# Kernel optimization log

Hardware: AMD Instinct MI355X
Metric: run time of the kernel (lower is better)

## Reference

```python
import jax, jax.numpy as jnp
import numpy as np

B, C, H, W = 4, 512, 96, 96
NH = 8
HD = C // NH
NC = 128
D = 768
L = H * W
EPS = 1e-5  # torch LayerNorm default


def _l2n(x, axis):
    # F.normalize: x / max(||x||, 1e-12)
    return x / jnp.maximum(jnp.linalg.norm(x, axis=axis, keepdims=True), 1e-12)


def _ln2d(x, g, b):
    # LayerNorm2d: normalize over channel dim of (B,C,H,W)
    mu = x.mean(1, keepdims=True)
    var = ((x - mu) ** 2).mean(1, keepdims=True)
    return (x - mu) / jnp.sqrt(var + EPS) * g[None, :, None, None] + b[None, :, None, None]


def _conv1x1(x, w):
    return jnp.einsum('oc,bchw->bohw', w, x)


def setup_inputs() -> dict:
    key = jax.random.key(0)
    ks = jax.random.split(key, 9)
    s = 0.02
    return {
        'img_feats': jax.random.normal(ks[0], (B, C, H, W), jnp.float32),
        'cls_embs': jax.random.normal(ks[1], (NC, D), jnp.float32),
        'cls_logits': jax.random.normal(ks[2], (B, NC), jnp.float32),
        'seg_logits': jax.random.normal(ks[3], (B, 1, H, W), jnp.float32),
        'gamma_g': jnp.ones((D,), jnp.float32), 'beta_g': jnp.zeros((D,), jnp.float32),
        'gamma_f': jnp.ones((C,), jnp.float32), 'beta_f': jnp.zeros((C,), jnp.float32),
        'attn_scale': jnp.ones((NH, 1, 1), jnp.float32),
        'Wg': jax.random.normal(ks[4], (C, D), jnp.float32) * s,
        'Wqkv': jax.random.normal(ks[5], (3 * C, C), jnp.float32) * s,
        'Wo': jax.random.normal(ks[6], (C, C), jnp.float32) * s,
        'bo': jnp.zeros((C,), jnp.float32),
        'gamma_n': jnp.ones((C,), jnp.float32), 'beta_n': jnp.zeros((C,), jnp.float32),
        'W1': jax.random.normal(ks[7], (C, C), jnp.float32) * s, 'b1': jnp.zeros((C,), jnp.float32),
        'W2': jax.random.normal(ks[8], (C, C), jnp.float32) * s, 'b2': jnp.zeros((C,), jnp.float32),
    }


def reference(img_feats, cls_embs, cls_logits, seg_logits, gamma_g, beta_g,
              gamma_f, beta_f, attn_scale, Wg, Wqkv, Wo, bo, gamma_n, beta_n,
              W1, b1, W2, b2):
    xn = _ln2d(img_feats, gamma_f, beta_f)
    # guide LayerNorm over embedding dim
    mu = cls_embs.mean(-1, keepdims=True)
    var = ((cls_embs - mu) ** 2).mean(-1, keepdims=True)
    cn = (cls_embs - mu) / jnp.sqrt(var + EPS) * gamma_g + beta_g
    g = (cn @ Wg.T).reshape(NC, NH, HD)  # nc nh hd

    qkv = _conv1x1(xn, Wqkv).reshape(B, 3, NH, HD, L)
    q, k, v = qkv[:, 0], qkv[:, 1], qkv[:, 2]  # each (B,NH,HD,L)

    # cosine guide map + min-max normalization + softmax-weighted aggregation over classes
    gm = jnp.einsum('nhd,bhdl->bhnl', _l2n(g, -1), _l2n(q, -2))
    gm = gm - gm.min(-1, keepdims=True)
    gm = gm / gm.max(-1, keepdims=True)
    gm = (jax.nn.softmax(gm, axis=2) * gm).sum(2, keepdims=True)  # (B,NH,1,L)

    # auxiliary guide map from cls logits + masked pooling of k
    cls_obj = jnp.einsum('nhd,bn->bhd', g, cls_logits)
    mask = jax.nn.sigmoid(seg_logits)  # (B,1,H,W)
    seg_obj = (mask * k.reshape(B, C, H, W)).sum((2, 3)) / mask.sum((2, 3))  # (B,C)
    obj = _l2n(cls_obj + seg_obj.reshape(B, NH, HD), -1)
    aux = jnp.einsum('bhd,bhdl->bhl', obj, _l2n(k, -2))[:, :, None, :]
    aux = aux - aux.min(-1, keepdims=True)
    aux = aux / aux.max(-1, keepdims=True)
    gm = gm * aux

    v = gm * v
    # channel (transposed) cosine attention: (B,NH,HD,HD)
    attn = jnp.einsum('bhdl,bhel->bhde', _l2n(q, -1), _l2n(k, -1)) * attn_scale
    out = jnp.einsum('bhde,bhel->bhdl', jax.nn.softmax(attn, -1), v).reshape(B, C, H, W)

    x = img_feats + _conv1x1(out, Wo) + bo[None, :, None, None]
    # ConvMlp with pre-norm: LayerNorm2d -> 1x1 conv -> GELU -> 1x1 conv
    fin = _ln2d(x, gamma_n, beta_n)
    h = jax.nn.gelu(_conv1x1(fin, W1) + b1[None, :, None, None], approximate=False)
    return x + _conv1x1(h, W2) + b2[None, :, None, None]
```

## Files before the change

### kernel.cpp

```cpp
#include <hip/hip_runtime.h>
#include <hip/hip_bf16.h>
#include <math.h>

#define BB 4
#define CC 512
#define NHEAD 8
#define HDIM 64
#define NCLS 128
#define DD 768
#define LL 9216
#define BLPIX 36864
#define EPSV 1e-5f
#define GMBLK 144
#define AUXBLK 36
#define LSPLIT 8
#define NLT 72

typedef __hip_bfloat16 bf16;
typedef __attribute__((ext_vector_type(8))) short short8v;
typedef __attribute__((ext_vector_type(4))) short short4v;
typedef __attribute__((ext_vector_type(4))) float f32x4;

__device__ __forceinline__ float bf2f(bf16 v){ return __bfloat162float(v); }
__device__ __forceinline__ bf16 f2bf(float v){ return __float2bfloat16(v); }
__device__ __forceinline__ short bfbits(float v){ bf16 b = __float2bfloat16(v); return *reinterpret_cast<short*>(&b); }
__device__ __forceinline__ float s2f(short s){ bf16 b = *reinterpret_cast<bf16*>(&s); return __bfloat162float(b); }

__global__ __launch_bounds__(256) void wclsg_k(
    const float* __restrict__ wqkv, const float* __restrict__ wo,
    const float* __restrict__ w1, const float* __restrict__ w2,
    bf16* __restrict__ oq, bf16* __restrict__ oo,
    bf16* __restrict__ o1, bf16* __restrict__ o2,
    const float* __restrict__ cls_embs, const float* __restrict__ gamma_g,
    const float* __restrict__ beta_g, const float* __restrict__ Wg,
    float* __restrict__ g, bf16* __restrict__ gnb)
{
  __shared__ __align__(16) float cn[DD];
  __shared__ float red[256];
  __shared__ float gsh[CC];
  __shared__ float nrm[NHEAD];
  int bid = blockIdx.x;
  int tid = threadIdx.x;
  if (bid < 1536){
    int i = bid * 256 + tid;
    int e = i * 4;
    const float* src; bf16* dst; int off;
    if (e < 786432){ src = wqkv; dst = oq; off = e; }
    else if (e < 1048576){ src = wo; dst = oo; off = e - 786432; }
    else if (e < 1310720){ src = w1; dst = o1; off = e - 1048576; }
    else { src = w2; dst = o2; off = e - 1310720; }
    float4 v = *reinterpret_cast<const float4*>(src + off);
    short4v pk;
    pk[0] = bfbits(v.x); pk[1] = bfbits(v.y); pk[2] = bfbits(v.z); pk[3] = bfbits(v.w);
    *(short4v*)&dst[off] = pk;
    return;
  }
  {
    int n = bid - 1536;
    const float* e = cls_embs + (size_t)n * DD;
    float s = 0.f, ss = 0.f;
    for (int i = tid; i < DD; i += 256){ float v = e[i]; s += v; ss += v * v; }
    red[tid] = s; __syncthreads();
    for (int st = 128; st > 0; st >>= 1){ if (tid < st) red[tid] += red[tid + st]; __syncthreads(); }
    float mean = red[0] / DD; __syncthreads();
    red[tid] = ss; __syncthreads();
    for (int st = 128; st > 0; st >>= 1){ if (tid < st) red[tid] += red[tid + st]; __syncthreads(); }
    float var = red[0] / DD - mean * mean;
    float rstd = rsqrtf(var + EPSV);
    __syncthreads();
    for (int i = tid; i < DD; i += 256) cn[i] = (e[i] - mean) * rstd * gamma_g[i] + beta_g[i];
    __syncthreads();
    for (int c = tid; c < CC; c += 256){
      const float* w = Wg + (size_t)c * DD;
      float a = 0.f;
      #pragma unroll 8
      for (int d = 0; d < DD; d++) a += cn[d] * w[d];
      gsh[c] = a;
    }
    __syncthreads();
    if (tid < NHEAD){
      float a = 0.f;
      for (int d = 0; d < HDIM; d++){ float v = gsh[tid * HDIM + d]; a += v * v; }
      nrm[tid] = fmaxf(sqrtf(a), 1e-12f);
    }
    __syncthreads();
    for (int c = tid; c < CC; c += 256){
      g[(size_t)n * CC + c] = gsh[c];
      gnb[(size_t)n * CC + c] = f2bf(gsh[c] / nrm[c >> 6]);
    }
  }
}

__global__ __launch_bounds__(256) void fuse_ln_k(const float* __restrict__ X,
    const float* __restrict__ lng, const float* __restrict__ lnb,
    bf16* __restrict__ xnT){
  __shared__ float sred[2][4][64];
  __shared__ float muS[64], rsS[64];
  __shared__ float t[64][65];
  int p0 = blockIdx.x * 64;
  int b = p0 / LL, l0 = p0 - b * LL;
  int tid = threadIdx.x;
  int cg = tid >> 6, l = tid & 63;
  const float* base = X + (size_t)b * CC * LL + l0 + l;
  float s = 0.f, ss = 0.f;
  for (int c = cg * 128; c < cg * 128 + 128; c++){
    float v = base[(size_t)c * LL];
    s += v; ss += v * v;
  }
  sred[0][cg][l] = s; sred[1][cg][l] = ss;
  __syncthreads();
  if (tid < 64){
    float st = sred[0][0][tid] + sred[0][1][tid] + sred[0][2][tid] + sred[0][3][tid];
    float sst = sred[1][0][tid] + sred[1][1][tid] + sred[1][2][tid] + sred[1][3][tid];
    float m = st * (1.0f / CC);
    float var = sst * (1.0f / CC) - m * m;
    muS[tid] = m; rsS[tid] = rsqrtf(var + EPSV);
  }
  __syncthreads();
  int pr = tid >> 4;
  int cc = (tid & 15) * 4;
  for (int cb = 0; cb < 8; cb++){
    int c0 = cb * 64;
    #pragma unroll
    for (int i = 0; i < 16; i++){
      int idx = i * 256 + tid;
      int cl = idx >> 6, ll2 = idx & 63;
      t[cl][ll2] = X[(size_t)b * CC * LL + (size_t)(c0 + cl) * LL + l0 + ll2];
    }
    __syncthreads();
    #pragma unroll
    for (int i = 0; i < 4; i++){
      int pl = pr + i * 16;
      int p = p0 + pl;
      float m = muS[pl], r = rsS[pl];
      short4v pk;
      #pragma unroll
      for (int e = 0; e < 4; e++){
        int c = c0 + cc + e;
        pk[e] = bfbits((t[cc + e][pl] - m) * r * lng[c] + lnb[c]);
      }
      *(short4v*)&xnT[(size_t)p * CC + c0 + cc] = pk;
    }
    __syncthreads();
  }
}

__global__ void statsred_k(const float2* __restrict__ statp, float* __restrict__ mu, float* __restrict__ rs){
  int p = blockIdx.x * 256 + threadIdx.x;
  if (p >= BLPIX) return;
  float s = 0.f, ss = 0.f;
  #pragma unroll
  for (int part = 0; part < 4; part++){
    float2 v = statp[part * BLPIX + p];
    s += v.x; ss += v.y;
  }
  float m = s * (1.0f / CC);
  float var = ss * (1.0f / CC) - m * m;
  mu[p] = m; rs[p] = rsqrtf(var + EPSV);
}

template<int MODE>
__global__ __launch_bounds__(256, 2) void mgemm_k(
    const bf16* __restrict__ A,
    const bf16* __restrict__ B,
    const float* __restrict__ residf,
    const bf16* __restrict__ residb,
    const float* __restrict__ bias,
    const float* __restrict__ mu, const float* __restrict__ rs,
    const float* __restrict__ lng, const float* __restrict__ lnb,
    float2* __restrict__ statp,
    float* __restrict__ qssp, float* __restrict__ kssp,
    bf16* __restrict__ qo, bf16* __restrict__ ko, bf16* __restrict__ vo,
    bf16* __restrict__ xT_out,
    float* __restrict__ xo,
    bf16* __restrict__ ho,
    const float* __restrict__ gA, const float* __restrict__ clsl, float* __restrict__ clsovO)
{
  __shared__ short Asm[128 * 64];
  __shared__ short Bsm[128 * 64];
  __shared__ float sredf[512];
  int tid = threadIdx.x;
  if (MODE == 0 && blockIdx.x >= 3456){
    int idx = (blockIdx.x - 3456) * 256 + tid;
    int b = idx >> 9, c = idx & 511;
    float a = 0.f;
    for (int n = 0; n < NCLS; n++) a += gA[(size_t)n * CC + c] * clsl[b * NCLS + n];
    clsovO[idx] = a;
    return;
  }
  int lane = tid & 63, wv = tid >> 6;
  int wr = wv >> 1, wc = wv & 1;
  int r15 = lane & 15, g = lane >> 4, h7 = lane & 7;
  int flat, gx, cpx;
  if (MODE == 0){ flat = blockIdx.x; gx = 12; cpx = 432; }
  else { gx = gridDim.x; flat = blockIdx.y * gx + blockIdx.x; cpx = (gx * gridDim.y) >> 3; }
  int swz = (flat & 7) * cpx + (flat >> 3);
  int m0 = (swz % gx) * 128, n0 = (swz / gx) * 128;
  int srow = tid >> 3, skkg = tid & 7;
  int sslot = ((skkg ^ (srow & 7))) * 8;

  f32x4 acc[4][4];
  #pragma unroll
  for (int i = 0; i < 4; i++)
    #pragma unroll
    for (int j = 0; j < 4; j++) acc[i][j] = (f32x4){0.f, 0.f, 0.f, 0.f};

  short8v pa[4], pb[4];
  auto loadAB = [&](int it){
    int k0 = it * 64;
    if (MODE == 2){
      int c0 = k0 + skkg * 8;
      float ga[8], be[8];
      *(float4*)&ga[0] = *(const float4*)&lng[c0];
      *(float4*)&ga[4] = *(const float4*)&lng[c0 + 4];
      *(float4*)&be[0] = *(const float4*)&lnb[c0];
      *(float4*)&be[4] = *(const float4*)&lnb[c0 + 4];
      #pragma unroll
      for (int r = 0; r < 4; r++){
        pa[r] = *reinterpret_cast<const short8v*>(A + (size_t)(m0 + r * 32 + srow) * 512 + c0);
        int rp = n0 + r * 32 + srow;
        float mm = mu[rp], rr = rs[rp];
        short8v rawv = *reinterpret_cast<const short8v*>(B + (size_t)rp * 512 + c0);
        short8v ov;
        #pragma unroll
        for (int e = 0; e < 8; e++){
          float v = (s2f(rawv[e]) - mm) * rr * ga[e] + be[e];
          ov[e] = bfbits(v);
        }
        pb[r] = ov;
      }
    } else {
      #pragma unroll
      for (int r = 0; r < 4; r++){
        pa[r] = *reinterpret_cast<const short8v*>(A + (size_t)(m0 + r * 32 + srow) * 512 + k0 + skkg * 8);
        pb[r] = *reinterpret_cast<const short8v*>(B + (size_t)(n0 + r * 32 + srow) * 512 + k0 + skkg * 8);
      }
    }
  };

  loadAB(0);
  for (int it = 0; it < 8; ++it){
    __syncthreads();
    #pragma unroll
    for (int r = 0; r < 4; r++){
      int row = r * 32 + srow;
      *(short8v*)&Asm[row * 64 + sslot] = pa[r];
      *(short8v*)&Bsm[row * 64 + sslot] = pb[r];
    }
    __syncthreads();
    if (it < 7) loadAB(it + 1);
    #pragma unroll
    for (int s = 0; s < 2; s++){
      int slot = ((s * 4 + g) ^ h7) * 8;
      short8v af[4], bf_[4];
      #pragma unroll
      for (int i = 0; i < 4; i++){
        af[i]  = *(const short8v*)&Asm[(wr * 64 + i * 16 + r15) * 64 + slot];
        bf_[i] = *(const short8v*)&Bsm[(wc * 64 + i * 16 + r15) * 64 + slot];
      }
      #pragma unroll
      for (int i = 0; i < 4; i++)
        #pragma unroll
        for (int j = 0; j < 4; j++){
          if (MODE == 2)
            acc[i][j] = __builtin_amdgcn_mfma_f32_16x16x32_bf16(bf_[i], af[j], acc[i][j], 0, 0, 0);
          else
            acc[i][j] = __builtin_amdgcn_mfma_f32_16x16x32_bf16(af[i], bf_[j], acc[i][j], 0, 0, 0);
        }
    }
  }

  int bIdx = n0 / LL;
  int lbase = n0 - bIdx * LL;
  if (MODE == 0){
    int part = m0 >> 9;
    if (part < 2){
      bf16* dst = (part == 0) ? qo : ko;
      int chb = (m0 & 511) + wr * 64;
      #pragma unroll
      for (int i = 0; i < 4; i++)
        #pragma unroll
        for (int j = 0; j < 4; j++){
          int l = lbase + wc * 64 + j * 16 + r15;
          #pragma unroll
          for (int e = 0; e < 4; e++){
            int ch = chb + i * 16 + g * 4 + e;
            dst[(size_t)bIdx * CC * LL + (size_t)ch * LL + l] = f2bf(acc[i][j][e]);
          }
        }
      #pragma unroll
      for (int i = 0; i < 4; i++)
        #pragma unroll
        for (int e = 0; e < 4; e++){
          float ssv = acc[i][0][e]*acc[i][0][e] + acc[i][1][e]*acc[i][1][e]
                    + acc[i][2][e]*acc[i][2][e] + acc[i][3][e]*acc[i][3][e];
          #pragma unroll
          for (int msk = 1; msk < 16; msk <<= 1) ssv += __shfl_xor(ssv, msk);
          if (r15 == 0) sredf[wv * 64 + i * 16 + g * 4 + e] = ssv;
        }
      __syncthreads();
      if (tid < 128){
        int wrr = tid >> 6, chL = tid & 63;
        float tot = sredf[(wrr * 2) * 64 + chL] + sredf[(wrr * 2 + 1) * 64 + chL];
        int c = (m0 & 511) + wrr * 64 + chL;
        int row = bIdx * 512 + c;
        int ltile = lbase >> 7;
        float* dd = (part == 0) ? qssp : kssp;
        dd[(size_t)row * NLT + ltile] = tot;
      }
    } else {
      int chb = (m0 & 511) + wr * 64;
      #pragma unroll
      for (int i = 0; i < 4; i++)
        #pragma unroll
        for (int j = 0; j < 4; j++){
          int l = lbase + wc * 64 + j * 16 + r15;
          int ch = chb + i * 16 + g * 4;
          short4v pk;
          #pragma unroll
          for (int e = 0; e < 4; e++) pk[e] = bfbits(acc[i][j][e]);
          *(short4v*)&vo[((size_t)bIdx * LL + l) * CC + ch] = pk;
        }
    }
  } else if (MODE == 1){
    float sj[4] = {0.f,0.f,0.f,0.f}, ssj[4] = {0.f,0.f,0.f,0.f};
    #pragma unroll
    for (int i = 0; i < 4; i++)
      #pragma unroll
      for (int j = 0; j < 4; j++){
        int l = lbase + wc * 64 + j * 16 + r15;
        int chm = m0 + wr * 64 + i * 16 + g * 4;
        short4v pk;
        #pragma unroll
        for (int e = 0; e < 4; e++){
          int m = chm + e;
          size_t o = (size_t)bIdx * CC * LL + (size_t)m * LL + l;
          float xv = residf[o] + acc[i][j][e] + bias[m];
          pk[e] = bfbits(xv);
          sj[j] += xv; ssj[j] += xv * xv;
        }
        *(short4v*)&xT_out[((size_t)bIdx * LL + l) * CC + chm] = pk;
      }
    #pragma unroll
    for (int j = 0; j < 4; j++){
      sj[j] += __shfl_xor(sj[j], 16); sj[j] += __shfl_xor(sj[j], 32);
      ssj[j] += __shfl_xor(ssj[j], 16); ssj[j] += __shfl_xor(ssj[j], 32);
    }
    if (g == 0){
      #pragma unroll
      for (int j = 0; j < 4; j++){
        sredf[wv * 128 + j * 32 + r15 * 2 + 0] = sj[j];
        sredf[wv * 128 + j * 32 + r15 * 2 + 1] = ssj[j];
      }
    }
    __syncthreads();
    if (tid < 128){
      int wv2 = tid >> 6, lane2 = tid & 63, j2 = lane2 >> 4, r2 = lane2 & 15;
      float s   = sredf[wv2 * 128 + j2 * 32 + r2 * 2 + 0] + sredf[(wv2 + 2) * 128 + j2 * 32 + r2 * 2 + 0];
      float ss2 = sredf[wv2 * 128 + j2 * 32 + r2 * 2 + 1] + sredf[(wv2 + 2) * 128 + j2 * 32 + r2 * 2 + 1];
      int p = n0 + wv2 * 64 + j2 * 16 + r2;
      statp[(m0 >> 7) * BLPIX + p] = make_float2(s, ss2);
    }
  } else if (MODE == 3){
    #pragma unroll
    for (int i = 0; i < 4; i++)
      #pragma unroll
      for (int j = 0; j < 4; j++){
        int l = lbase + wc * 64 + j * 16 + r15;
        int chm = m0 + wr * 64 + i * 16 + g * 4;
        short4v rv = *(const short4v*)&residb[((size_t)bIdx * LL + l) * CC + chm];
        #pragma unroll
        for (int e = 0; e < 4; e++){
          int m = chm + e;
          size_t o = (size_t)bIdx * CC * LL + (size_t)m * LL + l;
          xo[o] = s2f(rv[e]) + acc[i][j][e] + bias[m];
        }
      }
  } else {
    #pragma unroll
    for (int i = 0; i < 4; i++)
      #pragma unroll
      for (int j = 0; j < 4; j++){
        int mm = m0 + wr * 64 + j * 16 + r15;
        float bv = bias[mm];
        #pragma unroll
        for (int e = 0; e < 4; e++){
          int n = n0 + wc * 64 + i * 16 + g * 4 + e;
          float t = acc[i][j][e] + bv;
          float gv = 0.5f * t * (1.0f + erff(t * 0.70710678118654752f));
          ho[(size_t)n * CC + mm] = f2bf(gv);
        }
      }
  }
}

__global__ __launch_bounds__(256) void mega1_k(
    const bf16* __restrict__ q, const bf16* __restrict__ k, const bf16* __restrict__ gnb,
    float* __restrict__ pmin, float* __restrict__ pmax,
    float* __restrict__ part,
    const float* __restrict__ seg, float* __restrict__ seg_num, float* __restrict__ den,
    const float* __restrict__ qssp, const float* __restrict__ kssp,
    float* __restrict__ qn, float* __restrict__ kn)
{
  __shared__ __align__(16) char raw[9984];
  int bid = blockIdx.x;
  int t = threadIdx.x;
  if (bid < 4608){
    bf16* qs = (bf16*)raw;
    float (*sspart)[64] = (float(*)[64])(raw + 8704);
    float* rq = (float*)(raw + 8704 + 1024);
    int bh = bid & 31, lt = bid >> 5;
    int l0 = lt * 64;
    int b = bh >> 3, h = bh & 7;
    int w = t >> 6, lane = t & 63, r15 = lane & 15, g = lane >> 4;
    const bf16* qp = q + (size_t)b * CC * LL + (size_t)h * HDIM * LL + l0;
    #pragma unroll
    for (int i2 = 0; i2 < 4; i2++){
      int idx = t + i2 * 256;
      int d = idx >> 4, lch = (idx & 15) * 4;
      short4v vv = *reinterpret_cast<const short4v*>(qp + (size_t)d * LL + lch);
      *(short4v*)&qs[d * 68 + lch] = vv;
    }
    __syncthreads();
    {
      int l = t & 63, dg = t >> 6;
      float ss = 0.f;
      #pragma unroll
      for (int dd = 0; dd < 16; dd++){ float v = bf2f(qs[(dg * 16 + dd) * 68 + l]); ss += v * v; }
      sspart[dg][l] = ss;
    }
    __syncthreads();
    if (t < 64){
      float ss = sspart[0][t] + sspart[1][t] + sspart[2][t] + sspart[3][t];
      rq[t] = 1.0f / fmaxf(sqrtf(ss), 1e-12f);
    }
    __syncthreads();
    short8v ag[2][2];
    #pragma unroll
    for (int i = 0; i < 2; i++)
      #pragma unroll
      for (int kt = 0; kt < 2; kt++)
        ag[i][kt] = *reinterpret_cast<const short8v*>(gnb + (size_t)(w * 32 + i * 16 + r15) * CC + h * 64 + kt * 32 + g * 8);
    short8v bq[4][2];
    #pragma unroll
    for (int j = 0; j < 4; j++){
      float rqv = rq[j * 16 + r15];
      #pragma unroll
      for (int kt = 0; kt < 2; kt++){
        short8v bb;
        #pragma unroll
        for (int jj = 0; jj < 8; jj++){
          int d = kt * 32 + g * 8 + jj;
          bb[jj] = bfbits(bf2f(qs[d * 68 + j * 16 + r15]) * rqv);
        }
        bq[j][kt] = bb;
      }
    }
    f32x4 acc[2][4];
    #pragma unroll
    for (int i = 0; i < 2; i++)
      #pragma unroll
      for (int j = 0; j < 4; j++) acc[i][j] = (f32x4){0.f,0.f,0.f,0.f};
    #pragma unroll
    for (int kt = 0; kt < 2; kt++)
      #pragma unroll
      for (int i = 0; i < 2; i++)
        #pragma unroll
        for (int j = 0; j < 4; j++)
          acc[i][j] = __builtin_amdgcn_mfma_f32_16x16x32_bf16(ag[i][kt], bq[j][kt], acc[i][j], 0, 0, 0);
    #pragma unroll
    for (int i = 0; i < 2; i++)
      #pragma unroll
      for (int e = 0; e < 4; e++){
        float mn = acc[i][0][e], mx = acc[i][0][e];
        #pragma unroll
        for (int j = 1; j < 4; j++){ mn = fminf(mn, acc[i][j][e]); mx = fmaxf(mx, acc[i][j][e]); }
        #pragma unroll
        for (int msk = 1; msk < 16; msk <<= 1){
          mn = fminf(mn, __shfl_xor(mn, msk));
          mx = fmaxf(mx, __shfl_xor(mx, msk));
        }
        if (r15 == 0){
          int n = w * 32 + i * 16 + g * 4 + e;
          pmin[((size_t)bh * 128 + n) * GMBLK + lt] = mn;
          pmax[((size_t)bh * 128 + n) * GMBLK + lt] = mx;
        }
      }
    return;
  }
  if (bid < 4864){
    int bid2 = bid - 4608;
    int ls = bid2 & 7, bh = bid2 >> 3;
    int b = bh >> 3, h = bh & 7;
    int w = t >> 6, lane = t & 63, r15 = lane & 15, g = lane >> 4;
    const bf16* qp = q + (size_t)b * CC * LL + (size_t)h * HDIM * LL;
    const bf16* kp = k + (size_t)b * CC * LL + (size_t)h * HDIM * LL;
    int kbase = ls * 1152;
    f32x4 acc4[4];
    #pragma unroll
    for (int j = 0; j < 4; j++) acc4[j] = (f32x4){0.f,0.f,0.f,0.f};
    for (int ks = 0; ks < 36; ks++){
      int koff = kbase + ks * 32 + g * 8;
      short8v aq = *reinterpret_cast<const short8v*>(qp + (size_t)(w * 16 + r15) * LL + koff);
      short8v bk[4];
      #pragma unroll
      for (int j = 0; j < 4; j++) bk[j] = *reinterpret_cast<const short8v*>(kp + (size_t)(j * 16 + r15) * LL + koff);
      #pragma unroll
      for (int j = 0; j < 4; j++)
        acc4[j] = __builtin_amdgcn_mfma_f32_16x16x32_bf16(aq, bk[j], acc4[j], 0, 0, 0);
    }
    #pragma unroll
    for (int j = 0; j < 4; j++)
      #pragma unroll
      for (int e = 0; e < 4; e++){
        int d = w * 16 + g * 4 + e;
        int ee = j * 16 + r15;
        part[((size_t)(bh * LSPLIT + ls)) * 4096 + d * 64 + ee] = acc4[j][e];
      }
    return;
  }
  if (bid < 6912){
    float* red = (float*)raw;
    int bc = bid - 4864;
    int b = bc >> 9;
    const bf16* p = k + (size_t)bc * LL;
    const float* sp = seg + (size_t)b * LL;
    float s = 0.f;
    for (int i = t; i < LL; i += 256){
      float m = 1.0f / (1.0f + expf(-sp[i]));
      s += m * bf2f(p[i]);
    }
    red[t] = s; __syncthreads();
    for (int st = 128; st > 0; st >>= 1){ if (t < st) red[t] += red[t + st]; __syncthreads(); }
    if (t == 0) seg_num[bc] = red[0];
    return;
  }
  if (bid < 6916){
    float* red = (float*)raw;
    int b = bid - 6912;
    const float* sp = seg + (size_t)b * LL;
    float s = 0.f;
    for (int i = t; i < LL; i += 256) s += 1.0f / (1.0f + expf(-sp[i]));
    red[t] = s; __syncthreads();
    for (int st = 128; st > 0; st >>= 1){ if (t < st) red[t] += red[t + st]; __syncthreads(); }
    if (t == 0) den[b] = red[0];
    return;
  }
  {
    int r4 = (bid - 6916) * 4 + (t >> 6);
    int lane = t & 63;
    const float* src = (r4 < 2048) ? qssp : kssp;
    int r = r4 & 2047;
    float s = src[(size_t)r * NLT + lane] + ((lane < 8) ? src[(size_t)r * NLT + 64 + lane] : 0.f);
    #pragma unroll
    for (int m = 1; m < 64; m <<= 1) s += __shfl_xor(s, m);
    if (lane == 0){
      float nv = fmaxf(sqrtf(s), 1e-12f);
      if (r4 < 2048) qn[r] = nv; else kn[r] = nv;
    }
  }
}

__global__ void aux_k(const bf16* __restrict__ k,
                      const float* __restrict__ clsov, const float* __restrict__ segn,
                      const float* __restrict__ segd,
                      float* __restrict__ aux,
                      float* __restrict__ pmin, float* __restrict__ pmax){
  __shared__ float os[64];
  __shared__ float rmn[256], rmx[256];
  int bh = blockIdx.x, lt = blockIdx.y;
  int b = bh >> 3, h = bh & 7;
  int l = lt * 256 + threadIdx.x;
  if (threadIdx.x < 64){
    float sv = clsov[bh * 64 + threadIdx.x] + segn[bh * 64 + threadIdx.x] / segd[b];
    float ss = sv * sv;
    #pragma unroll
    for (int m = 1; m < 64; m <<= 1) ss += __shfl_xor(ss, m);
    os[threadIdx.x] = sv / fmaxf(sqrtf(ss), 1e-12f);
  }
  __syncthreads();
  const bf16* kp = k + (size_t)b * CC * LL + (size_t)h * HDIM * LL + l;
  float ss = 0.f, dot = 0.f;
  #pragma unroll 8
  for (int d = 0; d < 64; d++){ float v = bf2f(kp[(size_t)d * LL]); ss += v * v; dot += os[d] * v; }
  float av = dot / fmaxf(sqrtf(ss), 1e-12f);
  aux[(size_t)bh * LL + l] = av;
  rmn[threadIdx.x] = av; rmx[threadIdx.x] = av; __syncthreads();
  for (int st = 128; st > 0; st >>= 1){
    if (threadIdx.x < st){
      rmn[threadIdx.x] = fminf(rmn[threadIdx.x], rmn[threadIdx.x + st]);
      rmx[threadIdx.x] = fmaxf(rmx[threadIdx.x], rmx[threadIdx.x + st]);
    }
    __syncthreads();
  }
  if (threadIdx.x == 0){ pmin[bh * AUXBLK + lt] = rmn[0]; pmax[bh * AUXBLK + lt] = rmx[0]; }
}

__global__ __launch_bounds__(256) void megared_k(
    const float* __restrict__ gpmin, const float* __restrict__ gpmax,
    float* __restrict__ gmin, float* __restrict__ gms,
    const float* __restrict__ apmin, const float* __restrict__ apmax,
    float* __restrict__ amin, float* __restrict__ ams,
    const float* __restrict__ part, const float* __restrict__ qn,
    const float* __restrict__ kn, const float* __restrict__ scale,
    bf16* __restrict__ Pb)
{
  __shared__ float As[64 * 65];
  int bid = blockIdx.x;
  int tid = threadIdx.x;
  if (bid < 1024){
    int row = bid * 4 + (tid >> 6);
    int lane = tid & 63;
    float mn = gpmin[(size_t)row * GMBLK + lane];
    float mx = gpmax[(size_t)row * GMBLK + lane];
    mn = fminf(mn, gpmin[(size_t)row * GMBLK + 64 + lane]);
    mx = fmaxf(mx, gpmax[(size_t)row * GMBLK + 64 + lane]);
    if (lane < 16){
      mn = fminf(mn, gpmin[(size_t)row * GMBLK + 128 + lane]);
      mx = fmaxf(mx, gpmax[(size_t)row * GMBLK + 128 + lane]);
    }
    #pragma unroll
    for (int m = 1; m < 64; m <<= 1){
      mn = fminf(mn, __shfl_xor(mn, m));
      mx = fmaxf(mx, __shfl_xor(mx, m));
    }
    if (lane == 0){ gmin[row] = mn; gms[row] = mx - mn; }
    return;
  }
  if (bid < 1032){
    int bh = (bid - 1024) * 4 + (tid >> 6);
    int lane = tid & 63;
    float mn = (lane < AUXBLK) ? apmin[bh * AUXBLK + lane] : 1e30f;
    float mx = (lane < AUXBLK) ? apmax[bh * AUXBLK + lane] : -1e30f;
    #pragma unroll
    for (int m = 1; m < 64; m <<= 1){
      mn = fminf(mn, __shfl_xor(mn, m));
      mx = fmaxf(mx, __shfl_xor(mx, m));
    }
    if (lane == 0){ amin[bh] = mn; ams[bh] = mx - mn; }
    return;
  }
  {
    int bh = bid - 1032;
    int h = bh & 7;
    #pragma unroll
    for (int i = 0; i < 16; i++){
      int cell = tid + i * 256;
      int d = cell >> 6, e = cell & 63;
      float s = 0.f;
      #pragma unroll
      for (int ls = 0; ls < LSPLIT; ls++) s += part[((size_t)(bh * LSPLIT + ls)) * 4096 + cell];
      As[d * 65 + e] = s * scale[h] / (qn[bh * 64 + d] * kn[bh * 64 + e]);
    }
    __syncthreads();
    if (tid < 64){
      int d = tid;
      float mx = -1e30f;
      for (int e = 0; e < 64; e++) mx = fmaxf(mx, As[d * 65 + e]);
      float sum = 0.f;
      for (int e = 0; e < 64; e++){ float ev = expf(As[d * 65 + e] - mx); As[d * 65 + e] = ev; sum += ev; }
      float inv = 1.0f / sum;
      for (int e = 0; e < 64; e++) Pb[(size_t)bh * 4096 + d * 64 + e] = f2bf(As[d * 65 + e] * inv);
    }
  }
}

__global__ __launch_bounds__(256) void pv_k(const bf16* __restrict__ q, const bf16* __restrict__ gnb,
      const float* __restrict__ aux,
      const float* __restrict__ gmin, const float* __restrict__ gms,
      const float* __restrict__ amin, const float* __restrict__ ams,
      const bf16* __restrict__ Pb, const bf16* __restrict__ vT, bf16* __restrict__ outT){
  __shared__ bf16 qs[64 * 68];
  __shared__ float sspart[4][64];
  __shared__ float rq[64];
  __shared__ float gminS[128], rgmsS[128];
  __shared__ float separt[4][64], setpart[4][64];
  __shared__ float wl[64];
  int bh = blockIdx.x, lt = blockIdx.y;
  int l0 = lt * 64;
  int t = threadIdx.x;
  int b = bh >> 3, h = bh & 7;
  int w = t >> 6, lane = t & 63, r15 = lane & 15, g = lane >> 4;
  if (t < 128){ gminS[t] = gmin[bh * 128 + t]; rgmsS[t] = 1.0f / gms[bh * 128 + t]; }
  const bf16* qp = q + (size_t)b * CC * LL + (size_t)h * HDIM * LL + l0;
  #pragma unroll
  for (int i2 = 0; i2 < 4; i2++){
    int idx = t + i2 * 256;
    int d = idx >> 4, lch = (idx & 15) * 4;
    short4v vv = *reinterpret_cast<const short4v*>(qp + (size_t)d * LL + lch);
    *(short4v*)&qs[d * 68 + lch] = vv;
  }
  __syncthreads();
  {
    int l = t & 63, dg = t >> 6;
    float ss = 0.f;
    #pragma unroll
    for (int dd = 0; dd < 16; dd++){ float v = bf2f(qs[(dg * 16 + dd) * 68 + l]); ss += v * v; }
    sspart[dg][l] = ss;
  }
  __syncthreads();
  if (t < 64){
    float ss = sspart[0][t] + sspart[1][t] + sspart[2][t] + sspart[3][t];
    rq[t] = 1.0f / fmaxf(sqrtf(ss), 1e-12f);
  }
  __syncthreads();
  short8v ag[2][2];
  #pragma unroll
  for (int i = 0; i < 2; i++)
    #pragma unroll
    for (int kt = 0; kt < 2; kt++)
      ag[i][kt] = *reinterpret_cast<const short8v*>(gnb + (size_t)(w * 32 + i * 16 + r15) * CC + h * 64 + kt * 32 + g * 8);
  short8v bq[4][2];
  #pragma unroll
  for (int j = 0; j < 4; j++){
    float rqv = rq[j * 16 + r15];
    #pragma unroll
    for (int kt = 0; kt < 2; kt++){
      short8v bb;
      #pragma unroll
      for (int jj = 0; jj < 8; jj++){
        int d = kt * 32 + g * 8 + jj;
        bb[jj] = bfbits(bf2f(qs[d * 68 + j * 16 + r15]) * rqv);
      }
      bq[j][kt] = bb;
    }
  }
  f32x4 acc[2][4];
  #pragma unroll
  for (int i = 0; i < 2; i++)
    #pragma unroll
    for (int j = 0; j < 4; j++) acc[i][j] = (f32x4){0.f,0.f,0.f,0.f};
  #pragma unroll
  for (int kt = 0; kt < 2; kt++)
    #pragma unroll
    for (int i = 0; i < 2; i++)
      #pragma unroll
      for (int j = 0; j < 4; j++)
        acc[i][j] = __builtin_amdgcn_mfma_f32_16x16x32_bf16(ag[i][kt], bq[j][kt], acc[i][j], 0, 0, 0);
  float seL[4] = {0.f,0.f,0.f,0.f}, setL[4] = {0.f,0.f,0.f,0.f};
  #pragma unroll
  for (int i = 0; i < 2; i++)
    #pragma unroll
    for (int j = 0; j < 4; j++)
      #pragma unroll
      for (int e = 0; e < 4; e++){
        int n = w * 32 + i * 16 + g * 4 + e;
        float tt = (acc[i][j][e] - gminS[n]) * rgmsS[n];
        float ee = __expf(tt);
        seL[j] += ee; setL[j] += ee * tt;
      }
  #pragma unroll
  for (int j = 0; j < 4; j++){
    seL[j] += __shfl_xor(seL[j], 16); seL[j] += __shfl_xor(seL[j], 32);
    setL[j] += __shfl_xor(setL[j], 16); setL[j] += __shfl_xor(setL[j], 32);
  }
  if (g == 0){
    #pragma unroll
    for (int j = 0; j < 4; j++){ separt[w][j * 16 + r15] = seL[j]; setpart[w][j * 16 + r15] = setL[j]; }
  }
  __syncthreads();
  if (t < 64){
    float se = separt[0][t] + separt[1][t] + separt[2][t] + separt[3][t];
    float st = setpart[0][t] + setpart[1][t] + setpart[2][t] + setpart[3][t];
    float gmred = st / se;
    float auxn = (aux[(size_t)bh * LL + l0 + t] - amin[bh]) / ams[bh];
    wl[t] = gmred * auxn;
  }
  __syncthreads();
  short8v ap[4][2];
  #pragma unroll
  for (int i = 0; i < 4; i++)
    #pragma unroll
    for (int kt = 0; kt < 2; kt++)
      ap[i][kt] = *reinterpret_cast<const short8v*>(Pb + (size_t)bh * 4096 + (i * 16 + r15) * 64 + kt * 32 + g * 8);
  const bf16* vrow = vT + ((size_t)b * LL + l0 + w * 16 + r15) * CC + h * 64;
  short8v bv[2];
  #pragma unroll
  for (int kt = 0; kt < 2; kt++) bv[kt] = *reinterpret_cast<const short8v*>(vrow + kt * 32 + g * 8);
  f32x4 oacc[4];
  #pragma unroll
  for (int i = 0; i < 4; i++) oacc[i] = (f32x4){0.f,0.f,0.f,0.f};
  #pragma unroll
  for (int kt = 0; kt < 2; kt++)
    #pragma unroll
    for (int i = 0; i < 4; i++)
      oacc[i] = __builtin_amdgcn_mfma_f32_16x16x32_bf16(ap[i][kt], bv[kt], oacc[i], 0, 0, 0);
  float wlv = wl[w * 16 + r15];
  bf16* orow = outT + ((size_t)b * LL + l0 + w * 16 + r15) * CC + h * 64;
  #pragma unroll
  for (int i = 0; i < 4; i++){
    short4v pk;
    #pragma unroll
    for (int e = 0; e < 4; e++) pk[e] = bfbits(oacc[i][e] * wlv);
    *(short4v*)&orow[i * 16 + g * 4] = pk;
  }
}

extern "C" void kernel_launch(void* const* d_in, const int* in_sizes, int n_in,
                              void* d_out, int out_size, void* d_ws, size_t ws_size,
                              hipStream_t stream){
  const float* img        = (const float*)d_in[0];
  const float* cls_embs   = (const float*)d_in[1];
  const float* cls_logits = (const float*)d_in[2];
  const float* seg        = (const float*)d_in[3];
  const float* gamma_g    = (const float*)d_in[4];
  const float* beta_g     = (const float*)d_in[5];
  const float* gamma_f    = (const float*)d_in[6];
  const float* beta_f     = (const float*)d_in[7];
  const float* attn_scale = (const float*)d_in[8];
  const float* Wg         = (const float*)d_in[9];
  const float* Wqkv       = (const float*)d_in[10];
  const float* Wo         = (const float*)d_in[11];
  const float* bo         = (const float*)d_in[12];
  const float* gamma_n    = (const float*)d_in[13];
  const float* beta_n     = (const float*)d_in[14];
  const float* W1         = (const float*)d_in[15];
  const float* b1         = (const float*)d_in[16];
  const float* W2         = (const float*)d_in[17];
  const float* b2         = (const float*)d_in[18];
  float* outp = (float*)d_out;
  (void)in_sizes; (void)n_in; (void)out_size;

  char* wsb = (char*)d_ws;
  size_t off = 0;
  auto alloc = [&](size_t bytes)->char*{
    char* p = wsb + off;
    off += (bytes + 255) & ~(size_t)255;
    return p;
  };
  float* mu1   = (float*)alloc((size_t)BLPIX * 4);
  float* rs1   = (float*)alloc((size_t)BLPIX * 4);
  float2* statp= (float2*)alloc((size_t)4 * BLPIX * 8);
  float* qssp  = (float*)alloc((size_t)2048 * NLT * 4);
  float* kssp  = (float*)alloc((size_t)2048 * NLT * 4);
  float* qn    = (float*)alloc(2048 * 4);
  float* kn    = (float*)alloc(2048 * 4);
  float* gbuf  = (float*)alloc((size_t)NCLS * CC * 4);
  bf16*  gnbb  = (bf16*)alloc((size_t)NCLS * CC * 2);
  float* clsov = (float*)alloc(2048 * 4);
  float* segn  = (float*)alloc(2048 * 4);
  float* segd  = (float*)alloc(256);
  float* gminp = (float*)alloc((size_t)32 * 128 * GMBLK * 4);
  float* gmaxp = (float*)alloc((size_t)32 * 128 * GMBLK * 4);
  float* gminv = (float*)alloc(4096 * 4);
  float* gmsv  = (float*)alloc(4096 * 4);
  float* auxv  = (float*)alloc((size_t)32 * LL * 4);
  float* apmin = (float*)alloc(32 * AUXBLK * 4);
  float* apmax = (float*)alloc(32 * AUXBLK * 4);
  float* aminv = (float*)alloc(256);
  float* amsv  = (float*)alloc(256);
  bf16*  Pb    = (bf16*)alloc((size_t)32 * 4096 * 2);
  float* apart = (float*)alloc((size_t)32 * LSPLIT * 4096 * 4);
  bf16* qb    = (bf16*)alloc((size_t)BB * CC * LL * 2);
  bf16* kb    = (bf16*)alloc((size_t)BB * CC * LL * 2);
  bf16* wqkvb = (bf16*)alloc((size_t)1536 * 512 * 2);
  bf16* wob   = (bf16*)alloc((size_t)512 * 512 * 2);
  bf16* w1b   = (bf16*)alloc((size_t)512 * 512 * 2);
  bf16* w2b   = (bf16*)alloc((size_t)512 * 512 * 2);
  bf16* vT  = (bf16*)d_out;
  bf16* xnT = (bf16*)((char*)d_out + (size_t)BB * CC * LL * 2);
  bf16* outT = kb;
  bf16* xT   = qb;
  bf16* hbT  = kb;
  if (off > ws_size) return;

  wclsg_k<<<1664, 256, 0, stream>>>(Wqkv, Wo, W1, W2, wqkvb, wob, w1b, w2b,
      cls_embs, gamma_g, beta_g, Wg, gbuf, gnbb);
  fuse_ln_k<<<576, 256, 0, stream>>>(img, gamma_f, beta_f, xnT);
  mgemm_k<0><<<3464, 256, 0, stream>>>(wqkvb, xnT, nullptr, nullptr, nullptr,
      nullptr, nullptr, nullptr, nullptr, nullptr, qssp, kssp,
      qb, kb, vT, nullptr, nullptr, nullptr,
      gbuf, cls_logits, clsov);
  mega1_k<<<7940, 256, 0, stream>>>(qb, kb, gnbb, gminp, gmaxp, apart,
      seg, segn, segd, qssp, kssp, qn, kn);
  aux_k<<<dim3(32, AUXBLK), 256, 0, stream>>>(kb, clsov, segn, segd, auxv, apmin, apmax);
  megared_k<<<1064, 256, 0, stream>>>(gminp, gmaxp, gminv, gmsv,
      apmin, apmax, aminv, amsv,
      apart, qn, kn, attn_scale, Pb);
  pv_k<<<dim3(32, GMBLK), 256, 0, stream>>>(qb, gnbb, auxv, gminv, gmsv, aminv, amsv, Pb, vT, outT);
  mgemm_k<1><<<dim3(4, 288), 256, 0, stream>>>(wob, outT, img, nullptr, bo,
      nullptr, nullptr, nullptr, nullptr, statp, nullptr, nullptr,
      nullptr, nullptr, nullptr, xT, nullptr, nullptr,
      nullptr, nullptr, nullptr);
  statsred_k<<<144, 256, 0, stream>>>(statp, mu1, rs1);
  mgemm_k<2><<<dim3(4, 288), 256, 0, stream>>>(w1b, xT, nullptr, nullptr, b1,
      mu1, rs1, gamma_n, beta_n, nullptr, nullptr, nullptr,
      nullptr, nullptr, nullptr, nullptr, nullptr, hbT,
      nullptr, nullptr, nullptr);
  mgemm_k<3><<<dim3(4, 288), 256, 0, stream>>>(w2b, hbT, nullptr, xT, b2,
      nullptr, nullptr, nullptr, nullptr, nullptr, nullptr, nullptr,
      nullptr, nullptr, nullptr, nullptr, outp, nullptr,
      nullptr, nullptr, nullptr);
}
```

Measured before the change: 467.2 us.

## Precompute transposed q and its inverse norms once, reuse in guide-map kernels

Adds a qT_k kernel that transposes q into a pixel-major buffer and stores per-pixel inverse L2 norms. mega1_k and pv_k then load MFMA B-fragments straight from qT instead of each restaging q through shared memory, recomputing the norms and repacking to bf16. The norm scaling is now applied to the fp32 accumulators rather than to bf16 inputs, which changes rounding slightly. aux_k is also rebuilt to stage k tiles in LDS with 64-pixel blocks, so AUXBLK grows and the reduction in megared_k changes to match. The cost is an extra kernel launch plus a write and re-read of the full transposed q buffer.

```diff
diff --git a/kernel.cpp b/kernel.cpp
--- a/kernel.cpp
+++ b/kernel.cpp
@@ -12,7 +12,7 @@
 #define BLPIX 36864
 #define EPSV 1e-5f
 #define GMBLK 144
-#define AUXBLK 36
+#define AUXBLK 144
 #define LSPLIT 8
 #define NLT 72
 
@@ -145,6 +145,46 @@
   }
 }
 
+__global__ __launch_bounds__(256) void qT_k(const bf16* __restrict__ q,
+    bf16* __restrict__ qT, float* __restrict__ rq){
+  __shared__ bf16 qs[64 * 68];
+  __shared__ float sspart[4][64];
+  int bh = blockIdx.x, lt = blockIdx.y;
+  int l0 = lt * 64;
+  int t = threadIdx.x;
+  int b = bh >> 3, h = bh & 7;
+  const bf16* qp = q + (size_t)b * CC * LL + (size_t)h * HDIM * LL + l0;
+  #pragma unroll
+  for (int i2 = 0; i2 < 4; i2++){
+    int idx = t + i2 * 256;
+    int d = idx >> 4, lch = (idx & 15) * 4;
+    *(short4v*)&qs[d * 68 + lch] = *reinterpret_cast<const short4v*>(qp + (size_t)d * LL + lch);
+  }
+  __syncthreads();
+  {
+    int l = t & 63, dg = t >> 6;
+    float ss = 0.f;
+    #pragma unroll
+    for (int dd = 0; dd < 16; dd++){ float v = bf2f(qs[(dg * 16 + dd) * 68 + l]); ss += v * v; }
+    sspart[dg][l] = ss;
+  }
+  __syncthreads();
+  if (t < 64){
+    float ss = sspart[0][t] + sspart[1][t] + sspart[2][t] + sspart[3][t];
+    rq[(size_t)bh * LL + l0 + t] = 1.0f / fmaxf(sqrtf(ss), 1e-12f);
+  }
+  int px = t >> 2, d0 = (t & 3) * 16;
+  short8v o0, o1;
+  #pragma unroll
+  for (int jj = 0; jj < 8; jj++){
+    o0[jj] = *reinterpret_cast<short*>(&qs[(d0 + jj) * 68 + px]);
+    o1[jj] = *reinterpret_cast<short*>(&qs[(d0 + 8 + jj) * 68 + px]);
+  }
+  bf16* dst = qT + ((size_t)(b * LL + l0 + px)) * CC + h * 64 + d0;
+  *(short8v*)dst = o0;
+  *(short8v*)(dst + 8) = o1;
+}
+
 __global__ void statsred_k(const float2* __restrict__ statp, float* __restrict__ mu, float* __restrict__ rs){
   int p = blockIdx.x * 256 + threadIdx.x;
   if (p >= BLPIX) return;
@@ -396,65 +436,36 @@
 
 __global__ __launch_bounds__(256) void mega1_k(
     const bf16* __restrict__ q, const bf16* __restrict__ k, const bf16* __restrict__ gnb,
+    const bf16* __restrict__ qT, const float* __restrict__ rq,
     float* __restrict__ pmin, float* __restrict__ pmax,
     float* __restrict__ part,
     const float* __restrict__ seg, float* __restrict__ seg_num, float* __restrict__ den,
     const float* __restrict__ qssp, const float* __restrict__ kssp,
     float* __restrict__ qn, float* __restrict__ kn)
 {
-  __shared__ __align__(16) char raw[9984];
+  __shared__ __align__(16) float red[256];
   int bid = blockIdx.x;
   int t = threadIdx.x;
   if (bid < 4608){
-    bf16* qs = (bf16*)raw;
-    float (*sspart)[64] = (float(*)[64])(raw + 8704);
-    float* rq = (float*)(raw + 8704 + 1024);
     int bh = bid & 31, lt = bid >> 5;
     int l0 = lt * 64;
     int b = bh >> 3, h = bh & 7;
     int w = t >> 6, lane = t & 63, r15 = lane & 15, g = lane >> 4;
-    const bf16* qp = q + (size_t)b * CC * LL + (size_t)h * HDIM * LL + l0;
-    #pragma unroll
-    for (int i2 = 0; i2 < 4; i2++){
-      int idx = t + i2 * 256;
-      int d = idx >> 4, lch = (idx & 15) * 4;
-      short4v vv = *reinterpret_cast<const short4v*>(qp + (size_t)d * LL + lch);
-      *(short4v*)&qs[d * 68 + lch] = vv;
-    }
-    __syncthreads();
-    {
-      int l = t & 63, dg = t >> 6;
-      float ss = 0.f;
-      #pragma unroll
-      for (int dd = 0; dd < 16; dd++){ float v = bf2f(qs[(dg * 16 + dd) * 68 + l]); ss += v * v; }
-      sspart[dg][l] = ss;
-    }
-    __syncthreads();
-    if (t < 64){
-      float ss = sspart[0][t] + sspart[1][t] + sspart[2][t] + sspart[3][t];
-      rq[t] = 1.0f / fmaxf(sqrtf(ss), 1e-12f);
-    }
-    __syncthreads();
     short8v ag[2][2];
     #pragma unroll
     for (int i = 0; i < 2; i++)
       #pragma unroll
       for (int kt = 0; kt < 2; kt++)
         ag[i][kt] = *reinterpret_cast<const short8v*>(gnb + (size_t)(w * 32 + i * 16 + r15) * CC + h * 64 + kt * 32 + g * 8);
+    const bf16* qTp = qT + ((size_t)(b * LL + l0)) * CC + h * 64;
     short8v bq[4][2];
+    float rqv[4];
     #pragma unroll
     for (int j = 0; j < 4; j++){
-      float rqv = rq[j * 16 + r15];
-      #pragma unroll
-      for (int kt = 0; kt < 2; kt++){
-        short8v bb;
-        #pragma unroll
-        for (int jj = 0; jj < 8; jj++){
-          int d = kt * 32 + g * 8 + jj;
-          bb[jj] = bfbits(bf2f(qs[d * 68 + j * 16 + r15]) * rqv);
-        }
-        bq[j][kt] = bb;
-      }
+      #pragma unroll
+      for (int kt = 0; kt < 2; kt++)
+        bq[j][kt] = *reinterpret_cast<const short8v*>(qTp + (size_t)(j * 16 + r15) * CC + kt * 32 + g * 8);
+      rqv[j] = rq[(size_t)bh * LL + l0 + j * 16 + r15];
     }
     f32x4 acc[2][4];
     #pragma unroll
@@ -472,9 +483,12 @@
     for (int i = 0; i < 2; i++)
       #pragma unroll
       for (int e = 0; e < 4; e++){
-        float mn = acc[i][0][e], mx = acc[i][0][e];
-        #pragma unroll
-        for (int j = 1; j < 4; j++){ mn = fminf(mn, acc[i][j][e]); mx = fmaxf(mx, acc[i][j][e]); }
+        float mn = 1e30f, mx = -1e30f;
+        #pragma unroll
+        for (int j = 0; j < 4; j++){
+          float v = acc[i][j][e] * rqv[j];
+          mn = fminf(mn, v); mx = fmaxf(mx, v);
+        }
         #pragma unroll
         for (int msk = 1; msk < 16; msk <<= 1){
           mn = fminf(mn, __shfl_xor(mn, msk));
@@ -520,7 +534,6 @@
     return;
   }
   if (bid < 6912){
-    float* red = (float*)raw;
     int bc = bid - 4864;
     int b = bc >> 9;
     const bf16* p = k + (size_t)bc * LL;
@@ -536,7 +549,6 @@
     return;
   }
   if (bid < 6916){
-    float* red = (float*)raw;
     int b = bid - 6912;
     const float* sp = seg + (size_t)b * LL;
     float s = 0.f;
@@ -561,39 +573,57 @@
   }
 }
 
-__global__ void aux_k(const bf16* __restrict__ k,
+__global__ __launch_bounds__(256) void aux_k(const bf16* __restrict__ k,
                       const float* __restrict__ clsov, const float* __restrict__ segn,
                       const float* __restrict__ segd,
                       float* __restrict__ aux,
                       float* __restrict__ pmin, float* __restrict__ pmax){
+  __shared__ bf16 ks[64 * 68];
   __shared__ float os[64];
-  __shared__ float rmn[256], rmx[256];
+  __shared__ float sspart[4][64], dotpart[4][64];
   int bh = blockIdx.x, lt = blockIdx.y;
+  int l0 = lt * 64;
+  int t = threadIdx.x;
   int b = bh >> 3, h = bh & 7;
-  int l = lt * 256 + threadIdx.x;
-  if (threadIdx.x < 64){
-    float sv = clsov[bh * 64 + threadIdx.x] + segn[bh * 64 + threadIdx.x] / segd[b];
-    float ss = sv * sv;
-    #pragma unroll
-    for (int m = 1; m < 64; m <<= 1) ss += __shfl_xor(ss, m);
-    os[threadIdx.x] = sv / fmaxf(sqrtf(ss), 1e-12f);
+  const bf16* kp = k + (size_t)b * CC * LL + (size_t)h * HDIM * LL + l0;
+  #pragma unroll
+  for (int i2 = 0; i2 < 4; i2++){
+    int idx = t + i2 * 256;
+    int d = idx >> 4, lch = (idx & 15) * 4;
+    *(short4v*)&ks[d * 68 + lch] = *reinterpret_cast<const short4v*>(kp + (size_t)d * LL + lch);
+  }
+  if (t < 64){
+    float sv = clsov[bh * 64 + t] + segn[bh * 64 + t] / segd[b];
+    float ss2 = sv * sv;
+    #pragma unroll
+    for (int m = 1; m < 64; m <<= 1) ss2 += __shfl_xor(ss2, m);
+    os[t] = sv / fmaxf(sqrtf(ss2), 1e-12f);
   }
   __syncthreads();
-  const bf16* kp = k + (size_t)b * CC * LL + (size_t)h * HDIM * LL + l;
-  float ss = 0.f, dot = 0.f;
-  #pragma unroll 8
-  for (int d = 0; d < 64; d++){ float v = bf2f(kp[(size_t)d * LL]); ss += v * v; dot += os[d] * v; }
-  float av = dot / fmaxf(sqrtf(ss), 1e-12f);
-  aux[(size_t)bh * LL + l] = av;
-  rmn[threadIdx.x] = av; rmx[threadIdx.x] = av; __syncthreads();
-  for (int st = 128; st > 0; st >>= 1){
-    if (threadIdx.x < st){
-      rmn[threadIdx.x] = fminf(rmn[threadIdx.x], rmn[threadIdx.x + st]);
-      rmx[threadIdx.x] = fmaxf(rmx[threadIdx.x], rmx[threadIdx.x + st]);
-    }
-    __syncthreads();
-  }
-  if (threadIdx.x == 0){ pmin[bh * AUXBLK + lt] = rmn[0]; pmax[bh * AUXBLK + lt] = rmx[0]; }
+  {
+    int dg = t >> 6, l = t & 63;
+    float ssk = 0.f, dk = 0.f;
+    #pragma unroll
+    for (int dd = 0; dd < 16; dd++){
+      float v = bf2f(ks[(dg * 16 + dd) * 68 + l]);
+      ssk += v * v; dk += os[dg * 16 + dd] * v;
+    }
+    sspart[dg][l] = ssk; dotpart[dg][l] = dk;
+  }
+  __syncthreads();
+  if (t < 64){
+    float ss = sspart[0][t] + sspart[1][t] + sspart[2][t] + sspart[3][t];
+    float dot = dotpart[0][t] + dotpart[1][t] + dotpart[2][t] + dotpart[3][t];
+    float av = dot / fmaxf(sqrtf(ss), 1e-12f);
+    aux[(size_t)bh * LL + l0 + t] = av;
+    float mn = av, mx = av;
+    #pragma unroll
+    for (int m = 1; m < 64; m <<= 1){
+      mn = fminf(mn, __shfl_xor(mn, m));
+      mx = fmaxf(mx, __shfl_xor(mx, m));
+    }
+    if (t == 0){ pmin[bh * AUXBLK + lt] = mn; pmax[bh * AUXBLK + lt] = mx; }
+  }
 }
 
 __global__ __launch_bounds__(256) void megared_k(
@@ -630,8 +660,14 @@
   if (bid < 1032){
     int bh = (bid - 1024) * 4 + (tid >> 6);
     int lane = tid & 63;
-    float mn = (lane < AUXBLK) ? apmin[bh * AUXBLK + lane] : 1e30f;
-    float mx = (lane < AUXBLK) ? apmax[bh * AUXBLK + lane] : -1e30f;
+    float mn = apmin[bh * AUXBLK + lane];
+    float mx = apmax[bh * AUXBLK + lane];
+    mn = fminf(mn, apmin[bh * AUXBLK + 64 + lane]);
+    mx = fmaxf(mx, apmax[bh * AUXBLK + 64 + lane]);
+    if (lane < 16){
+      mn = fminf(mn, apmin[bh * AUXBLK + 128 + lane]);
+      mx = fmaxf(mx, apmax[bh * AUXBLK + 128 + lane]);
+    }
     #pragma unroll
     for (int m = 1; m < 64; m <<= 1){
       mn = fminf(mn, __shfl_xor(mn, m));
@@ -665,14 +701,12 @@
   }
 }
 
-__global__ __launch_bounds__(256) void pv_k(const bf16* __restrict__ q, const bf16* __restrict__ gnb,
+__global__ __launch_bounds__(256) void pv_k(const bf16* __restrict__ qT, const float* __restrict__ rq,
+      const bf16* __restrict__ gnb,
       const float* __restrict__ aux,
       const float* __restrict__ gmin, const float* __restrict__ gms,
       const float* __restrict__ amin, const float* __restrict__ ams,
       const bf16* __restrict__ Pb, const bf16* __restrict__ vT, bf16* __restrict__ outT){
-  __shared__ bf16 qs[64 * 68];
-  __shared__ float sspart[4][64];
-  __shared__ float rq[64];
   __shared__ float gminS[128], rgmsS[128];
   __shared__ float separt[4][64], setpart[4][64];
   __shared__ float wl[64];
@@ -682,48 +716,21 @@
   int b = bh >> 3, h = bh & 7;
   int w = t >> 6, lane = t & 63, r15 = lane & 15, g = lane >> 4;
   if (t < 128){ gminS[t] = gmin[bh * 128 + t]; rgmsS[t] = 1.0f / gms[bh * 128 + t]; }
-  const bf16* qp = q + (size_t)b * CC * LL + (size_t)h * HDIM * LL + l0;
-  #pragma unroll
-  for (int i2 = 0; i2 < 4; i2++){
-    int idx = t + i2 * 256;
-    int d = idx >> 4, lch = (idx & 15) * 4;
-    short4v vv = *reinterpret_cast<const short4v*>(qp + (size_t)d * LL + lch);
-    *(short4v*)&qs[d * 68 + lch] = vv;
-  }
-  __syncthreads();
-  {
-    int l = t & 63, dg = t >> 6;
-    float ss = 0.f;
-    #pragma unroll
-    for (int dd = 0; dd < 16; dd++){ float v = bf2f(qs[(dg * 16 + dd) * 68 + l]); ss += v * v; }
-    sspart[dg][l] = ss;
-  }
-  __syncthreads();
-  if (t < 64){
-    float ss = sspart[0][t] + sspart[1][t] + sspart[2][t] + sspart[3][t];
-    rq[t] = 1.0f / fmaxf(sqrtf(ss), 1e-12f);
-  }
-  __syncthreads();
   short8v ag[2][2];
   #pragma unroll
   for (int i = 0; i < 2; i++)
     #pragma unroll
     for (int kt = 0; kt < 2; kt++)
       ag[i][kt] = *reinterpret_cast<const short8v*>(gnb + (size_t)(w * 32 + i * 16 + r15) * CC + h * 64 + kt * 32 + g * 8);
+  const bf16* qTp = qT + ((size_t)(b * LL + l0)) * CC + h * 64;
   short8v bq[4][2];
+  float rqv[4];
   #pragma unroll
   for (int j = 0; j < 4; j++){
-    float rqv = rq[j * 16 + r15];
-    #pragma unroll
-    for (int kt = 0; kt < 2; kt++){
-      short8v bb;
-      #pragma unroll
-      for (int jj = 0; jj < 8; jj++){
-        int d = kt * 32 + g * 8 + jj;
-        bb[jj] = bfbits(bf2f(qs[d * 68 + j * 16 + r15]) * rqv);
-      }
-      bq[j][kt] = bb;
-    }
+    #pragma unroll
+    for (int kt = 0; kt < 2; kt++)
+      bq[j][kt] = *reinterpret_cast<const short8v*>(qTp + (size_t)(j * 16 + r15) * CC + kt * 32 + g * 8);
+    rqv[j] = rq[(size_t)bh * LL + l0 + j * 16 + r15];
   }
   f32x4 acc[2][4];
   #pragma unroll
@@ -737,6 +744,7 @@
       #pragma unroll
       for (int j = 0; j < 4; j++)
         acc[i][j] = __builtin_amdgcn_mfma_f32_16x16x32_bf16(ag[i][kt], bq[j][kt], acc[i][j], 0, 0, 0);
+  __syncthreads();
   float seL[4] = {0.f,0.f,0.f,0.f}, setL[4] = {0.f,0.f,0.f,0.f};
   #pragma unroll
   for (int i = 0; i < 2; i++)
@@ -745,7 +753,7 @@
       #pragma unroll
       for (int e = 0; e < 4; e++){
         int n = w * 32 + i * 16 + g * 4 + e;
-        float tt = (acc[i][j][e] - gminS[n]) * rgmsS[n];
+        float tt = (acc[i][j][e] * rqv[j] - gminS[n]) * rgmsS[n];
         float ee = __expf(tt);
         seL[j] += ee; setL[j] += ee * tt;
       }
@@ -835,6 +843,7 @@
   float* kssp  = (float*)alloc((size_t)2048 * NLT * 4);
   float* qn    = (float*)alloc(2048 * 4);
   float* kn    = (float*)alloc(2048 * 4);
+  float* rqb   = (float*)alloc((size_t)32 * LL * 4);
   float* gbuf  = (float*)alloc((size_t)NCLS * CC * 4);
   bf16*  gnbb  = (bf16*)alloc((size_t)NCLS * CC * 2);
   float* clsov = (float*)alloc(2048 * 4);
@@ -859,6 +868,7 @@
   bf16* w2b   = (bf16*)alloc((size_t)512 * 512 * 2);
   bf16* vT  = (bf16*)d_out;
   bf16* xnT = (bf16*)((char*)d_out + (size_t)BB * CC * LL * 2);
+  bf16* qTb = xnT;
   bf16* outT = kb;
   bf16* xT   = qb;
   bf16* hbT  = kb;
@@ -871,13 +881,14 @@
       nullptr, nullptr, nullptr, nullptr, nullptr, qssp, kssp,
       qb, kb, vT, nullptr, nullptr, nullptr,
       gbuf, cls_logits, clsov);
-  mega1_k<<<7940, 256, 0, stream>>>(qb, kb, gnbb, gminp, gmaxp, apart,
+  qT_k<<<dim3(32, 144), 256, 0, stream>>>(qb, qTb, rqb);
+  mega1_k<<<7940, 256, 0, stream>>>(qb, kb, gnbb, qTb, rqb, gminp, gmaxp, apart,
       seg, segn, segd, qssp, kssp, qn, kn);
-  aux_k<<<dim3(32, AUXBLK), 256, 0, stream>>>(kb, clsov, segn, segd, auxv, apmin, apmax);
+  aux_k<<<dim3(32, 144), 256, 0, stream>>>(kb, clsov, segn, segd, auxv, apmin, apmax);
   megared_k<<<1064, 256, 0, stream>>>(gminp, gmaxp, gminv, gmsv,
       apmin, apmax, aminv, amsv,
       apart, qn, kn, attn_scale, Pb);
-  pv_k<<<dim3(32, GMBLK), 256, 0, stream>>>(qb, gnbb, auxv, gminv, gmsv, aminv, amsv, Pb, vT, outT);
+  pv_k<<<dim3(32, GMBLK), 256, 0, stream>>>(qTb, rqb, gnbb, auxv, gminv, gmsv, aminv, amsv, Pb, vT, outT);
   mgemm_k<1><<<dim3(4, 288), 256, 0, stream>>>(wob, outT, img, nullptr, bo,
       nullptr, nullptr, nullptr, nullptr, statp, nullptr, nullptr,
       nullptr, nullptr, nullptr, xT, nullptr, nullptr,
```

New measurement: 485.7 us. 4.0% more time.
